# Optimization experiments

Measured on AMD Instinct MI355X. Metric: run time of the kernel, lower is better.

## Reference

```python
import jax, jax.numpy as jnp
import numpy as np

MAX_SCALE_CAP = 200
STEP = 3


def _shift(a, dy, dx):
    # a[..., y+dy, x+dx] with zero fill outside (dy, dx >= 0), matching the
    # zero-padded dilated 3x3 convs whose only off-center tap is at (+dy,+dx).
    H, W = a.shape[-2], a.shape[-1]
    p = jnp.pad(a, ((0, 0), (0, 0), (0, dy), (0, dx)))
    return p[..., dy:dy + H, dx:dx + W]


def _dif_stacks(Pred, GT, ROI):
    # Builds difPrd / difGT: channel order is (scale major, layer l, direction)
    # directions in dict order: Horizontal (0,+s), Vertical (+s,0), Diagonal (+s,+s)
    B, _, H, W = Pred.shape
    max_scale = min(MAX_SCALE_CAP, max(H, W))
    dP, dG = [], []
    for scale in range(1, max_scale, STEP):
        bP, bG = [], []
        for dy, dx in ((0, scale), (scale, 0), (scale, scale)):
            roi = ROI * _shift(ROI, dy, dx)             # [B,1,H,W]
            bP.append(roi * (Pred - _shift(Pred, dy, dx)))  # [B,3,H,W]
            bG.append(roi * (GT - _shift(GT, dy, dx)))
        # stack dirs on a new axis after layer axis -> l-major, dir-minor
        dP.append(jnp.stack(bP, axis=2).reshape(B, 9, H, W))
        dG.append(jnp.stack(bG, axis=2).reshape(B, 9, H, W))
    return jnp.concatenate(dP, axis=1), jnp.concatenate(dG, axis=1)


def _loss(PredXYZ, GTXYZ, ROIMask):
    difPrd, difGT = _dif_stacks(PredXYZ, GTXYZ, ROIMask)

    # normalization constant per image (detached in the original)
    Rat = jax.nn.relu(difPrd / (difGT + 1e-5))
    absG = jnp.abs(difGT)
    NormConst = (absG * Rat).sum((1, 2, 3)) / ((absG * (Rat > 0)).sum((1, 2, 3)) + 1e-4)
    NormConst = jax.lax.stop_gradient(NormConst)

    c = NormConst                                   # [B]
    safe_c = jnp.where(c > 1e-4, c, 1.0)
    term1 = jnp.where(
        c > 1e-4,
        jnp.abs(difGT - difPrd / safe_c[:, None, None, None]).mean((1, 2, 3)),
        0.0,
    )

    roi_sum = ROIMask.sum((1, 2, 3))
    pos_cnt = (difGT > 0).sum((1, 2, 3)).astype(jnp.float32)
    mean_prd = jnp.abs(difPrd).sum((1, 2, 3)) / pos_cnt

    big = roi_sum > 200
    term2 = jnp.where(big & (mean_prd > 30) & (c > 10), mean_prd - 30.0, 0.0)
    fact = 0.1 / (c + 0.001)
    term3 = jnp.where(big & (mean_prd < 2) & (c < 0.1), (0.2 - mean_prd) * fact, 0.0)

    return (term1 + term2 + term3).sum(), NormConst


def setup_inputs() -> dict:
    key = jax.random.key(0)
    k1, k2, k3 = jax.random.split(key, 3)
    PredXYZ = jax.random.normal(k1, (2, 3, 256, 256), dtype=jnp.float32)
    GTXYZ = jax.random.normal(k2, (2, 3, 256, 256), dtype=jnp.float32)
    ROIMask = (jax.random.uniform(k3, (2, 1, 256, 256)) > 0.3).astype(jnp.float32)
    return {"PredXYZ": PredXYZ, "GTXYZ": GTXYZ, "ROIMask": ROIMask}


def reference(PredXYZ, GTXYZ, ROIMask):
    return _loss(PredXYZ, GTXYZ, ROIMask)
```

## Files before the change

kernel.cpp:

```cpp
#include <hip/hip_runtime.h>


#define NSCALES 67
#define IMG_H 256
#define IMG_W 256
#define NPIX 65536
#define NLINES 2046
#define LMAX_PAD 320


__device__ __forceinline__ double wave_red(double v) {
#pragma unroll
  for (int o = 32; o > 0; o >>= 1) v += __shfl_down(v, o, 64);
  return v;
}

__device__ __forceinline__ void decode_line(int id, int& b, int& base, int& stride, int& L) {
  if (id < 512) {
    b = id >> 8; int y = id & 255;
    base = y * IMG_W; stride = 1; L = IMG_W;
  } else if (id < 1024) {
    int t = id - 512; b = t >> 8;
    base = t & 255; stride = IMG_W; L = IMG_H;
  } else {
    int t = id - 1024; b = (t >= 511) ? 1 : 0;
    int d = t - b * 511; int c = d - 255;
    int ac = (c < 0) ? -c : c;
    base = (c < 0) ? (-c) * IMG_W : c;
    stride = IMG_W + 1; L = 256 - ac;
  }
}

__device__ __forceinline__ int scale_count(int L, int q) {
  int rem = L - 1 - (q << 6);
  int kcnt = (rem >= 1) ? ((rem - 1) / 3 + 1) : 0;
  return (kcnt > NSCALES) ? NSCALES : kcnt;
}

__device__ __forceinline__ float stage_line(
    const float* __restrict__ Pred, const float* __restrict__ GT,
    const float* __restrict__ ROI, int b, int base, int stride, int L,
    int tid, float4* bufA, float4* bufB) {
  const float* P = Pred + b * (3 * NPIX);
  const float* G = GT + b * (3 * NPIX);
  const float* R = ROI + b * NPIX;
  float r = 0.f, p0 = 0.f, p1 = 0.f, p2 = 0.f, g0 = 0.f, g1 = 0.f, g2 = 0.f;
  if (tid < L) {
    int a = base + tid * stride;
    r = R[a];
    p0 = P[a]; p1 = P[a + NPIX]; p2 = P[a + 2 * NPIX];
    g0 = G[a]; g1 = G[a + NPIX]; g2 = G[a + 2 * NPIX];
  }
  bufA[tid] = make_float4(r, p0, p1, p2);
  bufB[tid] = make_float4(g0, g1, g2, 0.f);
  if (tid < LMAX_PAD - 256) {
    bufA[256 + tid] = make_float4(0.f, 0.f, 0.f, 0.f);
    bufB[256 + tid] = make_float4(0.f, 0.f, 0.f, 0.f);
  }
  __syncthreads();
  return r;
}

extern "C" __global__ void __launch_bounds__(256, 8) pass1_kernel(
    const float* __restrict__ Pred, const float* __restrict__ GT,
    const float* __restrict__ ROI, double* __restrict__ ws) {
  __shared__ float4 bufA[LMAX_PAD];
  __shared__ float4 bufB[LMAX_PAD];
  __shared__ double red[4][5];
  const int id = blockIdx.x;
  const int tid = threadIdx.x;
  const int wid = tid >> 6, lane = tid & 63;

  int b, base, stride, L;
  decode_line(id, b, base, stride, L);
  float stg_r = stage_line(Pred, GT, ROI, b, base, stride, L, tid, bufA, bufB);

  float f1 = 0.f, f2 = 0.f, fp = 0.f;
  int pci = 0;
  int P = 0;
  for (int q = 0; q < 4; ++q) {
    const int Kq = scale_count(L, q);
    int k = (wid - P) & 3;
    if (k < Kq) {
      const int c = (q << 6) + lane;
      const float4 cA = bufA[c];
      const float4 cB = bufB[c];
      const float cr = cA.x, cp0 = cA.y, cp1 = cA.z, cp2 = cA.w;
      const float cg0 = cB.x, cg1 = cB.y, cg2 = cB.z;
      const float4* tA = &bufA[c + 1 + 3 * k];
      const float4* tB = &bufB[c + 1 + 3 * k];
#pragma unroll 2
      for (; k < Kq; k += 4) {
        float4 t0 = tA[0];
        float4 t1 = tB[0];
        tA += 12; tB += 12;
        float rr = cr * t0.x;
#define L1BODY(cp, cg, tp, tg)                                   \
        {                                                        \
          float dP = rr * (cp - tp);                             \
          float dG = rr * (cg - tg);                             \
          float qq = dP * __builtin_amdgcn_rcpf(dG + 1e-5f);     \
          float aG = fabsf(dG);                                  \
          f1 += fmaxf(aG * qq, 0.f);                             \
          if (qq > 0.f) f2 += aG;                                \
          if (dG > 0.f) pci++;                                   \
          fp += fabsf(dP);                                       \
        }
        L1BODY(cp0, cg0, t0.y, t1.x)
        L1BODY(cp1, cg1, t0.z, t1.y)
        L1BODY(cp2, cg2, t0.w, t1.z)
#undef L1BODY
      }
    }
    P += Kq;
  }

  double w0 = wave_red((double)f1);
  double w1 = wave_red((double)f2);
  double w2 = wave_red((double)pci);
  double w3 = wave_red((double)fp);
  double w4 = wave_red((double)stg_r);
  if (lane == 0) {
    red[wid][0] = w0; red[wid][1] = w1; red[wid][2] = w2;
    red[wid][3] = w3; red[wid][4] = w4;
  }
  __syncthreads();
  if (tid < 4)
    unsafeAtomicAdd(&ws[b * 4 + tid],
                    red[0][tid] + red[1][tid] + red[2][tid] + red[3][tid]);
  if (tid == 4 && id < 512)
    unsafeAtomicAdd(&ws[8 + b], red[0][4] + red[1][4] + red[2][4] + red[3][4]);
}

extern "C" __global__ void __launch_bounds__(256, 8) pass2_kernel(
    const float* __restrict__ Pred, const float* __restrict__ GT,
    const float* __restrict__ ROI, double* __restrict__ ws) {
  __shared__ float4 bufA[LMAX_PAD];
  __shared__ float4 bufB[LMAX_PAD];
  __shared__ double red[4];
  __shared__ float s_invC;
  const int id = blockIdx.x;
  const int tid = threadIdx.x;
  const int wid = tid >> 6, lane = tid & 63;

  int b, base, stride, L;
  decode_line(id, b, base, stride, L);
  if (tid == 0) {
    double S1 = ws[b * 4 + 0], S2 = ws[b * 4 + 1];
    float cc = (float)(S1 / (S2 + 1e-4));
    s_invC = (cc > 1e-4f) ? (float)(1.0 / (double)cc) : 1.0f;
  }
  stage_line(Pred, GT, ROI, b, base, stride, L, tid, bufA, bufB);

  const float invC = s_invC;
  float f = 0.f;
  int P = 0;
  for (int q = 0; q < 4; ++q) {
    const int Kq = scale_count(L, q);
    int k = (wid - P) & 3;
    if (k < Kq) {
      const int c = (q << 6) + lane;
      const float4 cA = bufA[c];
      const float4 cB = bufB[c];
      const float cr = cA.x, cp0 = cA.y, cp1 = cA.z, cp2 = cA.w;
      const float cg0 = cB.x, cg1 = cB.y, cg2 = cB.z;
      const float4* tA = &bufA[c + 1 + 3 * k];
      const float4* tB = &bufB[c + 1 + 3 * k];
#pragma unroll 2
      for (; k < Kq; k += 4) {
        float4 t0 = tA[0];
        float4 t1 = tB[0];
        tA += 12; tB += 12;
        float rr = cr * t0.x;
        f += rr * fabsf((cg0 - t1.x) - (cp0 - t0.y) * invC);
        f += rr * fabsf((cg1 - t1.y) - (cp1 - t0.z) * invC);
        f += rr * fabsf((cg2 - t1.z) - (cp2 - t0.w) * invC);
      }
    }
    P += Kq;
  }
  double t = wave_red((double)f);
  if (lane == 0) red[wid] = t;
  __syncthreads();
  if (tid == 0)
    unsafeAtomicAdd(&ws[24 + b], red[0] + red[1] + red[2] + red[3]);
}

extern "C" __global__ void __launch_bounds__(64) final_kernel(
    const double* __restrict__ ws, float* __restrict__ out) {
  if (threadIdx.x == 0) {
    double loss = 0.0;
    for (int b = 0; b < 2; ++b) {
      double S1 = ws[b * 4 + 0], S2 = ws[b * 4 + 1];
      double PC = ws[b * 4 + 2], SP = ws[b * 4 + 3];
      double RS = ws[8 + b];
      float cc = (float)(S1 / (S2 + 1e-4));
      out[1 + b] = cc;
      double term1 = (cc > 1e-4f) ? ws[24 + b] / (603.0 * 65536.0) : 0.0;
      float meanPrd = (float)(SP / PC);
      bool big = RS > 200.0;
      float t2 = (big && meanPrd > 30.f && cc > 10.f) ? (meanPrd - 30.f) : 0.f;
      float fact = 0.1f / (cc + 0.001f);
      float t3 = (big && meanPrd < 2.f && cc < 0.1f) ? (0.2f - meanPrd) * fact : 0.f;
      loss += term1 + (double)(t2 + t3);
    }
    out[0] = (float)loss;
  }
}

extern "C" void kernel_launch(void* const* d_in, const int* in_sizes, int n_in,
                              void* d_out, int out_size, void* d_ws, size_t ws_size,
                              hipStream_t stream) {
  (void)in_sizes; (void)n_in; (void)out_size; (void)ws_size;
  const float* Pred = (const float*)d_in[0];
  const float* GT = (const float*)d_in[1];
  const float* ROI = (const float*)d_in[2];
  float* out = (float*)d_out;
  double* ws = (double*)d_ws;

  hipMemsetAsync(d_ws, 0, 32 * sizeof(double), stream);
  hipLaunchKernelGGL(pass1_kernel, dim3(NLINES), dim3(256), 0, stream,
                     Pred, GT, ROI, ws);
  hipLaunchKernelGGL(pass2_kernel, dim3(NLINES), dim3(256), 0, stream,
                     Pred, GT, ROI, ws);
  hipLaunchKernelGGL(final_kernel, dim3(1), dim3(64), 0, stream, ws, out);
}
```

Measured before the change: 128.3 us.

## Replace pass1 atomics with per-line partials and fold final kernel into pass2

Pass1 now writes per-block partial sums to distinct workspace slots instead of doing double atomics, and resets the pass2 accumulators itself, so the memset launch is dropped. Each pass2 block reduces the partials for its batch in one wavefront to get the normalization constant. The last-arriving pass2 block, found through an atomic counter, computes the final loss, which removes the separate final kernel launch. The cost is every pass2 block re-reading about 10k doubles of partials, plus a last-block counter protocol that relies on threadfence ordering.

```diff
diff --git a/kernel.cpp b/kernel.cpp
--- a/kernel.cpp
+++ b/kernel.cpp
@@ -8,6 +8,9 @@
 #define NLINES 2046
 #define LMAX_PAD 320
 
+#define T1_OFF 24
+#define CNT_OFF 26
+#define PART_OFF 32
 
 __device__ __forceinline__ double wave_red(double v) {
 #pragma unroll
@@ -31,6 +34,12 @@
   }
 }
 
+__device__ __forceinline__ int line_batch(int id) {
+  if (id < 512) return id >> 8;
+  if (id < 1024) return (id - 512) >> 8;
+  return (id - 1024) >= 511 ? 1 : 0;
+}
+
 __device__ __forceinline__ int scale_count(int L, int q) {
   int rem = L - 1 - (q << 6);
   int kcnt = (rem >= 1) ? ((rem - 1) / 3 + 1) : 0;
@@ -70,6 +79,12 @@
   const int id = blockIdx.x;
   const int tid = threadIdx.x;
   const int wid = tid >> 6, lane = tid & 63;
+
+  if (id == 0 && tid == 0) {
+    ws[T1_OFF + 0] = 0.0;
+    ws[T1_OFF + 1] = 0.0;
+    ((int*)&ws[CNT_OFF])[0] = 0;
+  }
 
   int b, base, stride, L;
   decode_line(id, b, base, stride, L);
@@ -119,40 +134,50 @@
   double w1 = wave_red((double)f2);
   double w2 = wave_red((double)pci);
   double w3 = wave_red((double)fp);
-  double w4 = wave_red((double)stg_r);
+  double w4 = wave_red((double)((id < 512) ? stg_r : 0.f));
   if (lane == 0) {
     red[wid][0] = w0; red[wid][1] = w1; red[wid][2] = w2;
     red[wid][3] = w3; red[wid][4] = w4;
   }
   __syncthreads();
-  if (tid < 4)
-    unsafeAtomicAdd(&ws[b * 4 + tid],
-                    red[0][tid] + red[1][tid] + red[2][tid] + red[3][tid]);
-  if (tid == 4 && id < 512)
-    unsafeAtomicAdd(&ws[8 + b], red[0][4] + red[1][4] + red[2][4] + red[3][4]);
+  if (tid < 5)
+    ws[PART_OFF + id * 5 + tid] =
+        red[0][tid] + red[1][tid] + red[2][tid] + red[3][tid];
 }
 
 extern "C" __global__ void __launch_bounds__(256, 8) pass2_kernel(
     const float* __restrict__ Pred, const float* __restrict__ GT,
-    const float* __restrict__ ROI, double* __restrict__ ws) {
+    const float* __restrict__ ROI, double* __restrict__ ws,
+    float* __restrict__ out) {
   __shared__ float4 bufA[LMAX_PAD];
   __shared__ float4 bufB[LMAX_PAD];
   __shared__ double red[4];
   __shared__ float s_invC;
+  __shared__ int s_isLast;
   const int id = blockIdx.x;
   const int tid = threadIdx.x;
   const int wid = tid >> 6, lane = tid & 63;
 
   int b, base, stride, L;
   decode_line(id, b, base, stride, L);
-  if (tid == 0) {
-    double S1 = ws[b * 4 + 0], S2 = ws[b * 4 + 1];
-    float cc = (float)(S1 / (S2 + 1e-4));
-    s_invC = (cc > 1e-4f) ? (float)(1.0 / (double)cc) : 1.0f;
-  }
   stage_line(Pred, GT, ROI, b, base, stride, L, tid, bufA, bufB);
 
+  if (wid == 0) {
+    double s1 = 0.0, s2 = 0.0;
+    for (int p = lane; p < NLINES; p += 64) {
+      bool mine = (line_batch(p) == b);
+      s1 += mine ? ws[PART_OFF + p * 5 + 0] : 0.0;
+      s2 += mine ? ws[PART_OFF + p * 5 + 1] : 0.0;
+    }
+    s1 = wave_red(s1); s2 = wave_red(s2);
+    if (lane == 0) {
+      float cc = (float)(s1 / (s2 + 1e-4));
+      s_invC = (cc > 1e-4f) ? (float)(1.0 / (double)cc) : 1.0f;
+    }
+  }
+  __syncthreads();
   const float invC = s_invC;
+
   float f = 0.f;
   int P = 0;
   for (int q = 0; q < 4; ++q) {
@@ -182,29 +207,51 @@
   double t = wave_red((double)f);
   if (lane == 0) red[wid] = t;
   __syncthreads();
-  if (tid == 0)
-    unsafeAtomicAdd(&ws[24 + b], red[0] + red[1] + red[2] + red[3]);
-}
-
-extern "C" __global__ void __launch_bounds__(64) final_kernel(
-    const double* __restrict__ ws, float* __restrict__ out) {
-  if (threadIdx.x == 0) {
-    double loss = 0.0;
-    for (int b = 0; b < 2; ++b) {
-      double S1 = ws[b * 4 + 0], S2 = ws[b * 4 + 1];
-      double PC = ws[b * 4 + 2], SP = ws[b * 4 + 3];
-      double RS = ws[8 + b];
-      float cc = (float)(S1 / (S2 + 1e-4));
-      out[1 + b] = cc;
-      double term1 = (cc > 1e-4f) ? ws[24 + b] / (603.0 * 65536.0) : 0.0;
-      float meanPrd = (float)(SP / PC);
-      bool big = RS > 200.0;
-      float t2 = (big && meanPrd > 30.f && cc > 10.f) ? (meanPrd - 30.f) : 0.f;
-      float fact = 0.1f / (cc + 0.001f);
-      float t3 = (big && meanPrd < 2.f && cc < 0.1f) ? (0.2f - meanPrd) * fact : 0.f;
-      loss += term1 + (double)(t2 + t3);
-    }
-    out[0] = (float)loss;
+  if (tid == 0) {
+    unsafeAtomicAdd(&ws[T1_OFF + b], red[0] + red[1] + red[2] + red[3]);
+    __threadfence();
+    int old = atomicAdd((int*)&ws[CNT_OFF], 1);
+    s_isLast = (old == NLINES - 1);
+  }
+  __syncthreads();
+
+  if (!s_isLast) return;
+
+  if (wid == 0) {
+    double a0[5] = {0, 0, 0, 0, 0}, a1[5] = {0, 0, 0, 0, 0};
+    for (int p = lane; p < NLINES; p += 64) {
+      bool b1 = (line_batch(p) == 1);
+#pragma unroll
+      for (int j = 0; j < 5; ++j) {
+        double v = ws[PART_OFF + p * 5 + j];
+        a0[j] += b1 ? 0.0 : v;
+        a1[j] += b1 ? v : 0.0;
+      }
+    }
+#pragma unroll
+    for (int j = 0; j < 5; ++j) { a0[j] = wave_red(a0[j]); a1[j] = wave_red(a1[j]); }
+    if (lane == 0) {
+      __threadfence();
+      double T1v[2];
+      T1v[0] = unsafeAtomicAdd(&ws[T1_OFF + 0], 0.0);
+      T1v[1] = unsafeAtomicAdd(&ws[T1_OFF + 1], 0.0);
+      double S1[2] = {a0[0], a1[0]}, S2[2] = {a0[1], a1[1]};
+      double PC[2] = {a0[2], a1[2]}, SP[2] = {a0[3], a1[3]};
+      double RS[2] = {a0[4], a1[4]};
+      double loss = 0.0;
+      for (int bb = 0; bb < 2; ++bb) {
+        float cc = (float)(S1[bb] / (S2[bb] + 1e-4));
+        out[1 + bb] = cc;
+        double term1 = (cc > 1e-4f) ? T1v[bb] / (603.0 * 65536.0) : 0.0;
+        float meanPrd = (float)(SP[bb] / PC[bb]);
+        bool big = RS[bb] > 200.0;
+        float t2 = (big && meanPrd > 30.f && cc > 10.f) ? (meanPrd - 30.f) : 0.f;
+        float fact = 0.1f / (cc + 0.001f);
+        float t3 = (big && meanPrd < 2.f && cc < 0.1f) ? (0.2f - meanPrd) * fact : 0.f;
+        loss += term1 + (double)(t2 + t3);
+      }
+      out[0] = (float)loss;
+    }
   }
 }
 
@@ -218,10 +265,8 @@
   float* out = (float*)d_out;
   double* ws = (double*)d_ws;
 
-  hipMemsetAsync(d_ws, 0, 32 * sizeof(double), stream);
   hipLaunchKernelGGL(pass1_kernel, dim3(NLINES), dim3(256), 0, stream,
                      Pred, GT, ROI, ws);
   hipLaunchKernelGGL(pass2_kernel, dim3(NLINES), dim3(256), 0, stream,
-                     Pred, GT, ROI, ws);
-  hipLaunchKernelGGL(final_kernel, dim3(1), dim3(64), 0, stream, ws, out);
-}
+                     Pred, GT, ROI, ws, out);
+}
```

Measured after the change: 162.1 us. +26.3%, slower.
